# Kernel optimization log

Measured on AMD Instinct MI355X. Metric: run time of the kernel, lower is better.

Reference implementation:

```python
import jax, jax.numpy as jnp
import numpy as np

LAMBDA_TEMPORAL = 0.5
LAMBDA_IDENTITY = 0.1
EPS = 1e-6


def setup_inputs() -> dict:
    key = jax.random.key(0)
    k1, k2, k3 = jax.random.split(key, 3)
    B, T, N = 16, 256, 2048
    pred_tracks_3d = jax.random.normal(k1, (B, T, N, 3), dtype=jnp.float32)
    gt_tracks_3d = jax.random.normal(k2, (B, T, N, 3), dtype=jnp.float32)
    gt_visibility = jax.random.uniform(k3, (B, T, N), dtype=jnp.float32)
    return {
        'pred_tracks_3d': pred_tracks_3d,
        'gt_tracks_3d': gt_tracks_3d,
        'gt_visibility': gt_visibility,
    }


def _compute_losses(pred, gt, vis):
    # visibility mask (B, T, N)
    m = (vis > 0.5).astype(pred.dtype)
    num_visible = jnp.sum(m)

    coord_w = jnp.array([1.0, 1.0, 2.0], dtype=pred.dtype)
    weighted_sq = jnp.square(pred - gt) * coord_w  # (B,T,N,3)
    recon = jnp.where(
        num_visible > 0,
        jnp.sum(weighted_sq * m[..., None]) / jnp.maximum(num_visible, 1.0),
        0.0,
    )

    # --- temporal: masked velocity MSE (visible in both adjacent frames) ---
    pred_vel = pred[:, 1:] - pred[:, :-1]
    gt_vel = gt[:, 1:] - gt[:, :-1]
    vel_mask = m[:, 1:] * m[:, :-1]  # (B,T-1,N)
    num_vel = jnp.sum(vel_mask)
    temporal = jnp.where(
        num_vel > 0,
        jnp.sum(jnp.square(pred_vel - gt_vel) * vel_mask[..., None]) / jnp.maximum(num_vel, 1.0),
        0.0,
    )

    # --- identity: per-point unbiased variance ratio over visible (b,t) samples ---
    n = jnp.sum(m, axis=(0, 1))  # (N,) visible count per point

    def masked_var(x):
        # unbiased (ddof=1) per-point, per-coord variance over masked (B,T) entries
        mean = jnp.einsum('btn,btnc->nc', m, x) / jnp.maximum(n, 1.0)[:, None]
        ss = jnp.einsum('btn,btnc->nc', m, jnp.square(x - mean[None, None]))
        return ss / jnp.maximum(n - 1.0, 1.0)[:, None]  # (N,3)

    pred_var = masked_var(pred)
    gt_var = masked_var(gt)
    var_ratio = jnp.sum(jnp.abs(pred_var - gt_var), axis=1) / (jnp.sum(gt_var, axis=1) + EPS)
    num_points = pred.shape[2]
    identity = jnp.sum(jnp.where(n > 1, var_ratio, 0.0)) / num_points

    # --- adaptive re-weighting (no-grad in original) ---
    rl = jax.lax.stop_gradient(recon)
    tl = jax.lax.stop_gradient(temporal)
    il = jax.lax.stop_gradient(identity)
    all_pos = (rl > 0) & (tl > 0) & (il > 0)
    max_comp = jnp.maximum(jnp.maximum(rl, tl), il)
    target = max_comp / 3.0
    thresh = 10.0 * target

    def adjust(base, comp):
        return jnp.where(all_pos & (comp > thresh), base * target / jnp.maximum(comp, 1e-30), base)

    rec_w = adjust(1.0, rl)
    temp_w = adjust(LAMBDA_TEMPORAL, tl)
    id_w = adjust(LAMBDA_IDENTITY, il)

    total = rec_w * recon + temp_w * temporal + id_w * identity
    return jnp.stack([total, recon, temporal, identity])


def reference(pred_tracks_3d, gt_tracks_3d, gt_visibility):
    # returns [total_loss, reconstruction_loss, temporal_loss, identity_loss]
    return _compute_losses(pred_tracks_3d, gt_tracks_3d, gt_visibility)
```

## Files before the change

### kernel.cpp

```cpp
#include <hip/hip_runtime.h>

#define BB 16
#define TT 256
#define NN 2048
#define TC 16
#define PD 4
#define NSLICE 16
#define WSBASE 64


__device__ __forceinline__ float waveReduceSum(float v) {
#pragma unroll
  for (int o = 32; o > 0; o >>= 1) v += __shfl_down(v, o, 64);
  return v;
}

__global__ __launch_bounds__(256, 6) void stats_kernel(
    const float* __restrict__ pred, const float* __restrict__ gt,
    const float* __restrict__ vis, float* __restrict__ ws) {
  const int n  = blockIdx.x * 256 + threadIdx.x;
  const int b  = blockIdx.y;
  const int t0 = blockIdx.z * TC;

  const size_t frame0 = (size_t)(b * TT + t0) * NN + n;
  const float3* __restrict__ pp = (const float3*)pred + frame0;
  const float3* __restrict__ gp = (const float3*)gt + frame0;
  const float*  __restrict__ vp = vis + frame0;

  float3 ppv, pgv;
  float mprev;
  {
    const long off = (t0 == 0) ? 0 : -(long)NN;
    ppv = pp[off];
    pgv = gp[off];
    float v = vp[off];
    mprev = (t0 != 0 && v > 0.5f) ? 1.f : 0.f;
  }

  float3 P[PD], G[PD];
  float  Vv[PD];
#pragma unroll
  for (int d = 0; d < PD; ++d) {
    P[d]  = pp[(size_t)d * NN];
    G[d]  = gp[(size_t)d * NN];
    Vv[d] = vp[(size_t)d * NN];
  }

  float cnt = 0.f;
  float sp0 = 0, sp1 = 0, sp2 = 0, qp0 = 0, qp1 = 0, qp2 = 0;
  float sg0 = 0, sg1 = 0, sg2 = 0, qg0 = 0, qg1 = 0, qg2 = 0;
  float recon = 0, temporal = 0, nvel = 0;

#pragma unroll
  for (int i = 0; i < TC; ++i) {
    const int sl = i & (PD - 1);
    float3 a = P[sl];
    float3 g = G[sl];
    float  v = Vv[sl];
    if (i + PD < TC) {
      P[sl]  = pp[(size_t)(i + PD) * NN];
      G[sl]  = gp[(size_t)(i + PD) * NN];
      Vv[sl] = vp[(size_t)(i + PD) * NN];
    }
    float m = (v > 0.5f) ? 1.f : 0.f;

    cnt += m;
    sp0 += m * a.x; sp1 += m * a.y; sp2 += m * a.z;
    qp0 += m * a.x * a.x; qp1 += m * a.y * a.y; qp2 += m * a.z * a.z;
    sg0 += m * g.x; sg1 += m * g.y; sg2 += m * g.z;
    qg0 += m * g.x * g.x; qg1 += m * g.y * g.y; qg2 += m * g.z * g.z;
    float d0 = a.x - g.x, d1 = a.y - g.y, d2 = a.z - g.z;
    recon += m * (d0 * d0 + d1 * d1 + 2.f * d2 * d2);

    float mv = m * mprev;
    float vx = (a.x - ppv.x) - (g.x - pgv.x);
    float vy = (a.y - ppv.y) - (g.y - pgv.y);
    float vz = (a.z - ppv.z) - (g.z - pgv.z);
    temporal += mv * (vx * vx + vy * vy + vz * vz);
    nvel += mv;

    ppv = a; pgv = g; mprev = m;
  }

  const int slice = (b + 2 * blockIdx.z) & (NSLICE - 1);
  float* pts = ws + WSBASE + (size_t)slice * 13 * NN;
  atomicAdd(&pts[0 * NN + n], cnt);
  atomicAdd(&pts[1 * NN + n], sp0);
  atomicAdd(&pts[2 * NN + n], sp1);
  atomicAdd(&pts[3 * NN + n], sp2);
  atomicAdd(&pts[4 * NN + n], qp0);
  atomicAdd(&pts[5 * NN + n], qp1);
  atomicAdd(&pts[6 * NN + n], qp2);
  atomicAdd(&pts[7 * NN + n], sg0);
  atomicAdd(&pts[8 * NN + n], sg1);
  atomicAdd(&pts[9 * NN + n], sg2);
  atomicAdd(&pts[10 * NN + n], qg0);
  atomicAdd(&pts[11 * NN + n], qg1);
  atomicAdd(&pts[12 * NN + n], qg2);

  __shared__ float sred[3][4];
  float r0 = waveReduceSum(recon);
  float r1 = waveReduceSum(temporal);
  float r2 = waveReduceSum(nvel);
  int lane = threadIdx.x & 63, w = threadIdx.x >> 6;
  if (lane == 0) { sred[0][w] = r0; sred[1][w] = r1; sred[2][w] = r2; }
  __syncthreads();
  if (threadIdx.x < 3) {
    float s = sred[threadIdx.x][0] + sred[threadIdx.x][1] +
              sred[threadIdx.x][2] + sred[threadIdx.x][3];
    atomicAdd(&ws[slice * 3 + threadIdx.x], s);
  }
}

__global__ __launch_bounds__(256) void identity_kernel(float* __restrict__ ws,
                                                       float* __restrict__ out) {
  const int n = blockIdx.x * 256 + threadIdx.x;
  const float* base = ws + WSBASE;
  float st[13];
#pragma unroll
  for (int k = 0; k < 13; ++k) st[k] = 0.f;
#pragma unroll
  for (int s = 0; s < NSLICE; ++s) {
#pragma unroll
    for (int k = 0; k < 13; ++k) st[k] += base[(size_t)(s * 13 + k) * NN + n];
  }
  float c = st[0];
  float sp0 = st[1], sp1 = st[2], sp2 = st[3];
  float qp0 = st[4], qp1 = st[5], qp2 = st[6];
  float sg0 = st[7], sg1 = st[8], sg2 = st[9];
  float qg0 = st[10], qg1 = st[11], qg2 = st[12];

  float inv = 1.f / fmaxf(c, 1.f);
  float dv  = 1.f / fmaxf(c - 1.f, 1.f);
  float pv0 = (qp0 - sp0 * sp0 * inv) * dv;
  float pv1 = (qp1 - sp1 * sp1 * inv) * dv;
  float pv2 = (qp2 - sp2 * sp2 * inv) * dv;
  float gv0 = (qg0 - sg0 * sg0 * inv) * dv;
  float gv1 = (qg1 - sg1 * sg1 * inv) * dv;
  float gv2 = (qg2 - sg2 * sg2 * inv) * dv;

  float num = fabsf(pv0 - gv0) + fabsf(pv1 - gv1) + fabsf(pv2 - gv2);
  float den = gv0 + gv1 + gv2 + 1e-6f;
  float contrib = (c > 1.f) ? (num / den) : 0.f;

  __shared__ float sred[2][4];
  float r0 = waveReduceSum(contrib);
  float r1 = waveReduceSum(c);
  int lane = threadIdx.x & 63, w = threadIdx.x >> 6;
  if (lane == 0) { sred[0][w] = r0; sred[1][w] = r1; }
  __syncthreads();
  if (threadIdx.x < 2) {
    float s = sred[threadIdx.x][0] + sred[threadIdx.x][1] +
              sred[threadIdx.x][2] + sred[threadIdx.x][3];
    atomicAdd(&ws[48 + threadIdx.x], s);
  }

  __threadfence();
  __shared__ int isLast;
  if (threadIdx.x == 0) {
    int old = atomicAdd((int*)(ws + 50), 1);
    isLast = (old == (int)gridDim.x - 1) ? 1 : 0;
  }
  __syncthreads();
  if (isLast && threadIdx.x < 64) {
    float r = 0.f, t = 0.f, v = 0.f;
    if (lane < NSLICE) {
      r = atomicAdd(&ws[lane * 3 + 0], 0.f);
      t = atomicAdd(&ws[lane * 3 + 1], 0.f);
      v = atomicAdd(&ws[lane * 3 + 2], 0.f);
    }
    r = waveReduceSum(r);
    t = waveReduceSum(t);
    v = waveReduceSum(v);
    if (lane == 0) {
      float idsum = atomicAdd(&ws[48], 0.f);
      float nvis  = atomicAdd(&ws[49], 0.f);
      float recon = (nvis > 0.f) ? r / fmaxf(nvis, 1.f) : 0.f;
      float temporal = (v > 0.f) ? t / fmaxf(v, 1.f) : 0.f;
      float identity = idsum / (float)NN;

      float rl = recon, tl = temporal, il = identity;
      bool all_pos = (rl > 0.f) && (tl > 0.f) && (il > 0.f);
      float maxc = fmaxf(rl, fmaxf(tl, il));
      float target = maxc / 3.f;
      float thresh = 10.f * target;
      float rw = (all_pos && rl > thresh) ? 1.0f * target / fmaxf(rl, 1e-30f) : 1.0f;
      float tw = (all_pos && tl > thresh) ? 0.5f * target / fmaxf(tl, 1e-30f) : 0.5f;
      float iw = (all_pos && il > thresh) ? 0.1f * target / fmaxf(il, 1e-30f) : 0.1f;

      out[0] = rw * recon + tw * temporal + iw * identity;
      out[1] = recon;
      out[2] = temporal;
      out[3] = identity;
    }
  }
}

extern "C" void kernel_launch(void* const* d_in, const int* in_sizes, int n_in,
                              void* d_out, int out_size, void* d_ws, size_t ws_size,
                              hipStream_t stream) {
  const float* pred = (const float*)d_in[0];
  const float* gt   = (const float*)d_in[1];
  const float* vis  = (const float*)d_in[2];
  float* out = (float*)d_out;
  float* ws  = (float*)d_ws;

  hipMemsetAsync(d_ws, 0, (WSBASE + (size_t)NSLICE * 13 * NN) * sizeof(float), stream);

  dim3 g1(NN / 256, BB, TT / TC);
  stats_kernel<<<g1, 256, 0, stream>>>(pred, gt, vis, ws);
  identity_kernel<<<dim3(NN / 256), 256, 0, stream>>>(ws, out);
}
```

Measured before the change: 256.3 us.

## Replace per-point atomics with plain partial stores plus a separate reduction pass

When workspace is large enough, each stats block writes its 13 per-point partial sums to its own region with plain stores instead of atomically adding into 16 shared slices. A new reduce kernel sums the 256 regions per statistic into a compact buffer, which the identity kernel then reads. The memset shrinks to the header only, the manual register prefetch pipeline is removed, and the occupancy hint rises from 6 to 8. The cost is roughly 27 MB of extra partial-sum traffic and one more kernel launch, in exchange for removing atomic contention and the large memset.

```diff
diff --git a/kernel.cpp b/kernel.cpp
--- a/kernel.cpp
+++ b/kernel.cpp
@@ -4,9 +4,11 @@
 #define TT 256
 #define NN 2048
 #define TC 16
-#define PD 4
+#define NREG (BB * (TT / TC))
 #define NSLICE 16
-#define WSBASE 64
+#define HDR 64
+#define COMPACT HDR
+#define REGION (HDR + 13 * NN)
 
 
 __device__ __forceinline__ float waveReduceSum(float v) {
@@ -15,7 +17,8 @@
   return v;
 }
 
-__global__ __launch_bounds__(256, 6) void stats_kernel(
+template <bool STORE>
+__global__ __launch_bounds__(256, 8) void stats_kernel(
     const float* __restrict__ pred, const float* __restrict__ gt,
     const float* __restrict__ vis, float* __restrict__ ws) {
   const int n  = blockIdx.x * 256 + threadIdx.x;
@@ -26,6 +29,11 @@
   const float3* __restrict__ pp = (const float3*)pred + frame0;
   const float3* __restrict__ gp = (const float3*)gt + frame0;
   const float*  __restrict__ vp = vis + frame0;
+
+  float cnt = 0.f;
+  float sp0 = 0, sp1 = 0, sp2 = 0, qp0 = 0, qp1 = 0, qp2 = 0;
+  float sg0 = 0, sg1 = 0, sg2 = 0, qg0 = 0, qg1 = 0, qg2 = 0;
+  float recon = 0, temporal = 0, nvel = 0;
 
   float3 ppv, pgv;
   float mprev;
@@ -37,31 +45,11 @@
     mprev = (t0 != 0 && v > 0.5f) ? 1.f : 0.f;
   }
 
-  float3 P[PD], G[PD];
-  float  Vv[PD];
-#pragma unroll
-  for (int d = 0; d < PD; ++d) {
-    P[d]  = pp[(size_t)d * NN];
-    G[d]  = gp[(size_t)d * NN];
-    Vv[d] = vp[(size_t)d * NN];
-  }
-
-  float cnt = 0.f;
-  float sp0 = 0, sp1 = 0, sp2 = 0, qp0 = 0, qp1 = 0, qp2 = 0;
-  float sg0 = 0, sg1 = 0, sg2 = 0, qg0 = 0, qg1 = 0, qg2 = 0;
-  float recon = 0, temporal = 0, nvel = 0;
-
 #pragma unroll
   for (int i = 0; i < TC; ++i) {
-    const int sl = i & (PD - 1);
-    float3 a = P[sl];
-    float3 g = G[sl];
-    float  v = Vv[sl];
-    if (i + PD < TC) {
-      P[sl]  = pp[(size_t)(i + PD) * NN];
-      G[sl]  = gp[(size_t)(i + PD) * NN];
-      Vv[sl] = vp[(size_t)(i + PD) * NN];
-    }
+    float3 a = pp[(size_t)i * NN];
+    float3 g = gp[(size_t)i * NN];
+    float v = vp[(size_t)i * NN];
     float m = (v > 0.5f) ? 1.f : 0.f;
 
     cnt += m;
@@ -82,21 +70,25 @@
     ppv = a; pgv = g; mprev = m;
   }
 
-  const int slice = (b + 2 * blockIdx.z) & (NSLICE - 1);
-  float* pts = ws + WSBASE + (size_t)slice * 13 * NN;
-  atomicAdd(&pts[0 * NN + n], cnt);
-  atomicAdd(&pts[1 * NN + n], sp0);
-  atomicAdd(&pts[2 * NN + n], sp1);
-  atomicAdd(&pts[3 * NN + n], sp2);
-  atomicAdd(&pts[4 * NN + n], qp0);
-  atomicAdd(&pts[5 * NN + n], qp1);
-  atomicAdd(&pts[6 * NN + n], qp2);
-  atomicAdd(&pts[7 * NN + n], sg0);
-  atomicAdd(&pts[8 * NN + n], sg1);
-  atomicAdd(&pts[9 * NN + n], sg2);
-  atomicAdd(&pts[10 * NN + n], qg0);
-  atomicAdd(&pts[11 * NN + n], qg1);
-  atomicAdd(&pts[12 * NN + n], qg2);
+  if (STORE) {
+    const int r = b * (TT / TC) + blockIdx.z;
+    float* pts = ws + REGION + (size_t)r * 13 * NN + n;
+    pts[0 * NN]  = cnt;
+    pts[1 * NN]  = sp0;  pts[2 * NN]  = sp1;  pts[3 * NN]  = sp2;
+    pts[4 * NN]  = qp0;  pts[5 * NN]  = qp1;  pts[6 * NN]  = qp2;
+    pts[7 * NN]  = sg0;  pts[8 * NN]  = sg1;  pts[9 * NN]  = sg2;
+    pts[10 * NN] = qg0;  pts[11 * NN] = qg1;  pts[12 * NN] = qg2;
+  } else {
+    const int r = (b + 2 * blockIdx.z) & (NSLICE - 1);
+    float* pts = ws + REGION + (size_t)r * 13 * NN + n;
+    atomicAdd(&pts[0 * NN], cnt);
+    atomicAdd(&pts[1 * NN], sp0);  atomicAdd(&pts[2 * NN], sp1);
+    atomicAdd(&pts[3 * NN], sp2);  atomicAdd(&pts[4 * NN], qp0);
+    atomicAdd(&pts[5 * NN], qp1);  atomicAdd(&pts[6 * NN], qp2);
+    atomicAdd(&pts[7 * NN], sg0);  atomicAdd(&pts[8 * NN], sg1);
+    atomicAdd(&pts[9 * NN], sg2);  atomicAdd(&pts[10 * NN], qg0);
+    atomicAdd(&pts[11 * NN], qg1); atomicAdd(&pts[12 * NN], qg2);
+  }
 
   __shared__ float sred[3][4];
   float r0 = waveReduceSum(recon);
@@ -108,22 +100,35 @@
   if (threadIdx.x < 3) {
     float s = sred[threadIdx.x][0] + sred[threadIdx.x][1] +
               sred[threadIdx.x][2] + sred[threadIdx.x][3];
+    const int slice = (b + 2 * blockIdx.z) & (NSLICE - 1);
     atomicAdd(&ws[slice * 3 + threadIdx.x], s);
   }
 }
 
-__global__ __launch_bounds__(256) void identity_kernel(float* __restrict__ ws,
-                                                       float* __restrict__ out) {
+template <int NR>
+__global__ __launch_bounds__(256) void reduce_kernel(float* __restrict__ ws) {
+  const int idx = blockIdx.x * 256 + threadIdx.x;
+  const int n = idx & (NN - 1);
+  const int k = idx >> 11;
+  const float* src = ws + REGION + (size_t)k * NN + n;
+  float s0 = 0.f, s1 = 0.f, s2 = 0.f, s3 = 0.f;
+#pragma unroll 8
+  for (int r = 0; r < NR; r += 4) {
+    s0 += src[(size_t)(r + 0) * 13 * NN];
+    s1 += src[(size_t)(r + 1) * 13 * NN];
+    s2 += src[(size_t)(r + 2) * 13 * NN];
+    s3 += src[(size_t)(r + 3) * 13 * NN];
+  }
+  ws[COMPACT + (size_t)k * NN + n] = (s0 + s1) + (s2 + s3);
+}
+
+__global__ __launch_bounds__(256) void identity_final(float* __restrict__ ws,
+                                                      float* __restrict__ out) {
   const int n = blockIdx.x * 256 + threadIdx.x;
-  const float* base = ws + WSBASE;
   float st[13];
 #pragma unroll
-  for (int k = 0; k < 13; ++k) st[k] = 0.f;
-#pragma unroll
-  for (int s = 0; s < NSLICE; ++s) {
-#pragma unroll
-    for (int k = 0; k < 13; ++k) st[k] += base[(size_t)(s * 13 + k) * NN + n];
-  }
+  for (int k = 0; k < 13; ++k) st[k] = ws[COMPACT + (size_t)k * NN + n];
+
   float c = st[0];
   float sp0 = st[1], sp1 = st[2], sp2 = st[3];
   float qp0 = st[4], qp1 = st[5], qp2 = st[6];
@@ -205,9 +210,20 @@
   float* out = (float*)d_out;
   float* ws  = (float*)d_ws;
 
-  hipMemsetAsync(d_ws, 0, (WSBASE + (size_t)NSLICE * 13 * NN) * sizeof(float), stream);
-
   dim3 g1(NN / 256, BB, TT / TC);
-  stats_kernel<<<g1, 256, 0, stream>>>(pred, gt, vis, ws);
-  identity_kernel<<<dim3(NN / 256), 256, 0, stream>>>(ws, out);
-}
+  const size_t need_store =
+      (size_t)(REGION + (size_t)NREG * 13 * NN) * sizeof(float);
+
+  if (ws_size >= need_store) {
+    hipMemsetAsync(d_ws, 0, HDR * sizeof(float), stream);
+    stats_kernel<true><<<g1, 256, 0, stream>>>(pred, gt, vis, ws);
+    reduce_kernel<NREG><<<dim3(13 * NN / 256), 256, 0, stream>>>(ws);
+  } else {
+    hipMemsetAsync(d_ws, 0,
+                   (size_t)(REGION + (size_t)NSLICE * 13 * NN) * sizeof(float),
+                   stream);
+    stats_kernel<false><<<g1, 256, 0, stream>>>(pred, gt, vis, ws);
+    reduce_kernel<NSLICE><<<dim3(13 * NN / 256), 256, 0, stream>>>(ws);
+  }
+  identity_final<<<dim3(NN / 256), 256, 0, stream>>>(ws, out);
+}
```

New measurement: 272.6 us. 1.06x slower.

## Stage pred/gt tiles through LDS with async global_load_lds and halve time chunk

Applied to the files above, without the earlier changes.

The stats kernel now stages pred and gt tiles for 8 frames into shared memory using direct global-to-LDS 16-byte loads. This replaces per-thread strided float3 register loads with coalesced wide transfers, and uses explicit vmcnt waits so compute on frame s can overlap the loads still in flight. The time chunk per block is halved, which doubles the grid and the number of atomic partial-sum writes, and the occupancy hint is dropped. The temporal term is reformulated to reuse the pred-gt difference, and the slice mapping for atomics changes.

```diff
diff --git a/kernel.cpp b/kernel.cpp
--- a/kernel.cpp
+++ b/kernel.cpp
@@ -3,11 +3,14 @@
 #define BB 16
 #define TT 256
 #define NN 2048
-#define TC 16
-#define PD 4
+#define TC 8
 #define NSLICE 16
-#define WSBASE 64
-
+#define HDR 64
+#define PTS HDR
+
+
+typedef const __attribute__((address_space(1))) void* gas1_t;
+typedef __attribute__((address_space(3))) void* las3_t;
 
 __device__ __forceinline__ float waveReduceSum(float v) {
 #pragma unroll
@@ -15,35 +18,49 @@
   return v;
 }
 
-__global__ __launch_bounds__(256, 6) void stats_kernel(
+__global__ __launch_bounds__(256) void stats_kernel(
     const float* __restrict__ pred, const float* __restrict__ gt,
     const float* __restrict__ vis, float* __restrict__ ws) {
-  const int n  = blockIdx.x * 256 + threadIdx.x;
-  const int b  = blockIdx.y;
-  const int t0 = blockIdx.z * TC;
-
-  const size_t frame0 = (size_t)(b * TT + t0) * NN + n;
-  const float3* __restrict__ pp = (const float3*)pred + frame0;
-  const float3* __restrict__ gp = (const float3*)gt + frame0;
-  const float*  __restrict__ vp = vis + frame0;
-
-  float3 ppv, pgv;
-  float mprev;
+  __shared__ float sP[TC * 768];
+  __shared__ float sG[TC * 768];
+
+  const int tid  = threadIdx.x;
+  const int w    = tid >> 6;
+  const int lane = tid & 63;
+  const int n0   = blockIdx.x * 256;
+  const int b    = blockIdx.y;
+  const int t0   = blockIdx.z * TC;
+  const int tb   = (t0 == 0) ? 0 : t0 - 1;
+
+  const size_t elemB = (size_t)(b * TT + tb) * NN + n0 + tid;
+  float3 ab = *(const float3*)(pred + elemB * 3);
+  float3 gb = *(const float3*)(gt   + elemB * 3);
+  float  vb = vis[elemB];
+
+  const size_t elem0 = (size_t)(b * TT + t0) * NN + n0 + tid;
+  float vv[TC];
+#pragma unroll
+  for (int s = 0; s < TC; ++s) vv[s] = vis[elem0 + (size_t)s * NN];
+
+  asm volatile("s_waitcnt vmcnt(0)" ::: "memory");
+  __builtin_amdgcn_sched_barrier(0);
+
+  float mprev = (t0 != 0 && vb > 0.5f) ? 1.f : 0.f;
+  float epx = ab.x - gb.x, epy = ab.y - gb.y, epz = ab.z - gb.z;
+
   {
-    const long off = (t0 == 0) ? 0 : -(long)NN;
-    ppv = pp[off];
-    pgv = gp[off];
-    float v = vp[off];
-    mprev = (t0 != 0 && v > 0.5f) ? 1.f : 0.f;
-  }
-
-  float3 P[PD], G[PD];
-  float  Vv[PD];
-#pragma unroll
-  for (int d = 0; d < PD; ++d) {
-    P[d]  = pp[(size_t)d * NN];
-    G[d]  = gp[(size_t)d * NN];
-    Vv[d] = vp[(size_t)d * NN];
+    const size_t fbase = ((size_t)(b * TT + t0) * NN + n0) * 3;
+    const float* pf = pred + fbase + w * 192 + lane * 4;
+    const float* gf = gt   + fbase + w * 192 + lane * 4;
+    if (lane < 48) {
+#pragma unroll
+      for (int s = 0; s < TC; ++s) {
+        __builtin_amdgcn_global_load_lds((gas1_t)(pf + (size_t)s * NN * 3),
+                                         (las3_t)&sP[s * 768 + w * 192], 16, 0, 0);
+        __builtin_amdgcn_global_load_lds((gas1_t)(gf + (size_t)s * NN * 3),
+                                         (las3_t)&sG[s * 768 + w * 192], 16, 0, 0);
+      }
+    }
   }
 
   float cnt = 0.f;
@@ -52,38 +69,32 @@
   float recon = 0, temporal = 0, nvel = 0;
 
 #pragma unroll
-  for (int i = 0; i < TC; ++i) {
-    const int sl = i & (PD - 1);
-    float3 a = P[sl];
-    float3 g = G[sl];
-    float  v = Vv[sl];
-    if (i + PD < TC) {
-      P[sl]  = pp[(size_t)(i + PD) * NN];
-      G[sl]  = gp[(size_t)(i + PD) * NN];
-      Vv[sl] = vp[(size_t)(i + PD) * NN];
-    }
-    float m = (v > 0.5f) ? 1.f : 0.f;
-
+  for (int s = 0; s < TC; ++s) {
+    asm volatile("s_waitcnt vmcnt(%0)" :: "i"(2 * TC - 2 - 2 * s) : "memory");
+    __builtin_amdgcn_sched_barrier(0);
+    float3 a = *(const float3*)&sP[s * 768 + tid * 3];
+    float3 g = *(const float3*)&sG[s * 768 + tid * 3];
+    float m = (vv[s] > 0.5f) ? 1.f : 0.f;
+
+    float ex = a.x - g.x, ey = a.y - g.y, ez = a.z - g.z;
     cnt += m;
     sp0 += m * a.x; sp1 += m * a.y; sp2 += m * a.z;
     qp0 += m * a.x * a.x; qp1 += m * a.y * a.y; qp2 += m * a.z * a.z;
     sg0 += m * g.x; sg1 += m * g.y; sg2 += m * g.z;
     qg0 += m * g.x * g.x; qg1 += m * g.y * g.y; qg2 += m * g.z * g.z;
-    float d0 = a.x - g.x, d1 = a.y - g.y, d2 = a.z - g.z;
-    recon += m * (d0 * d0 + d1 * d1 + 2.f * d2 * d2);
+    recon += m * (ex * ex + ey * ey + 2.f * ez * ez);
 
     float mv = m * mprev;
-    float vx = (a.x - ppv.x) - (g.x - pgv.x);
-    float vy = (a.y - ppv.y) - (g.y - pgv.y);
-    float vz = (a.z - ppv.z) - (g.z - pgv.z);
-    temporal += mv * (vx * vx + vy * vy + vz * vz);
+    float dx = ex - epx, dy = ey - epy, dz = ez - epz;
+    temporal += mv * (dx * dx + dy * dy + dz * dz);
     nvel += mv;
 
-    ppv = a; pgv = g; mprev = m;
-  }
-
-  const int slice = (b + 2 * blockIdx.z) & (NSLICE - 1);
-  float* pts = ws + WSBASE + (size_t)slice * 13 * NN;
+    epx = ex; epy = ey; epz = ez; mprev = m;
+  }
+
+  const int slice = (b + blockIdx.z) & (NSLICE - 1);
+  float* pts = ws + PTS + (size_t)slice * 13 * NN;
+  const int n = n0 + tid;
   atomicAdd(&pts[0 * NN + n], cnt);
   atomicAdd(&pts[1 * NN + n], sp0);
   atomicAdd(&pts[2 * NN + n], sp1);
@@ -102,20 +113,18 @@
   float r0 = waveReduceSum(recon);
   float r1 = waveReduceSum(temporal);
   float r2 = waveReduceSum(nvel);
-  int lane = threadIdx.x & 63, w = threadIdx.x >> 6;
   if (lane == 0) { sred[0][w] = r0; sred[1][w] = r1; sred[2][w] = r2; }
   __syncthreads();
-  if (threadIdx.x < 3) {
-    float s = sred[threadIdx.x][0] + sred[threadIdx.x][1] +
-              sred[threadIdx.x][2] + sred[threadIdx.x][3];
-    atomicAdd(&ws[slice * 3 + threadIdx.x], s);
-  }
-}
-
-__global__ __launch_bounds__(256) void identity_kernel(float* __restrict__ ws,
-                                                       float* __restrict__ out) {
+  if (tid < 3) {
+    float s = sred[tid][0] + sred[tid][1] + sred[tid][2] + sred[tid][3];
+    atomicAdd(&ws[slice * 3 + tid], s);
+  }
+}
+
+__global__ __launch_bounds__(256) void identity_final(float* __restrict__ ws,
+                                                      float* __restrict__ out) {
   const int n = blockIdx.x * 256 + threadIdx.x;
-  const float* base = ws + WSBASE;
+  const float* base = ws + PTS;
   float st[13];
 #pragma unroll
   for (int k = 0; k < 13; ++k) st[k] = 0.f;
@@ -205,9 +214,11 @@
   float* out = (float*)d_out;
   float* ws  = (float*)d_ws;
 
-  hipMemsetAsync(d_ws, 0, (WSBASE + (size_t)NSLICE * 13 * NN) * sizeof(float), stream);
+  hipMemsetAsync(d_ws, 0,
+                 (size_t)(HDR + (size_t)NSLICE * 13 * NN) * sizeof(float),
+                 stream);
 
   dim3 g1(NN / 256, BB, TT / TC);
   stats_kernel<<<g1, 256, 0, stream>>>(pred, gt, vis, ws);
-  identity_kernel<<<dim3(NN / 256), 256, 0, stream>>>(ws, out);
-}
+  identity_final<<<dim3(NN / 256), 256, 0, stream>>>(ws, out);
+}
```

Result: no change. 253.3 us (-1.2%).
